# Kernel tuning notes

Hardware: AMD Instinct MI355X
Metric: run time of the kernel (lower is better)

## Reference

```python
import jax, jax.numpy as jnp
import numpy as np

D_MODEL = 768
H = 12
D_K = D_MODEL // H
NEG = -1e9


def setup_inputs() -> dict:
    key = jax.random.key(0)
    ks = jax.random.split(key, 12)
    B, S = 1, 4096
    q = jax.random.normal(ks[0], (B, S, D_MODEL), dtype=jnp.float32)
    k = jax.random.normal(ks[1], (B, S, D_MODEL), dtype=jnp.float32)
    v = jax.random.normal(ks[2], (B, S, D_MODEL), dtype=jnp.float32)
    # causal mask, 1 = attend, 0 = masked (masked_fill on mask == 0)
    mask = jnp.tril(jnp.ones((S, S), dtype=jnp.int32))[None, None, :, :]
    scale = 1.0 / np.sqrt(D_MODEL)
    Wq = jax.random.normal(ks[3], (D_MODEL, D_MODEL), dtype=jnp.float32) * scale
    bq = jnp.zeros((D_MODEL,), dtype=jnp.float32)
    Wk = jax.random.normal(ks[4], (D_MODEL, D_MODEL), dtype=jnp.float32) * scale
    bk = jnp.zeros((D_MODEL,), dtype=jnp.float32)
    Wv = jax.random.normal(ks[5], (D_MODEL, D_MODEL), dtype=jnp.float32) * scale
    bv = jnp.zeros((D_MODEL,), dtype=jnp.float32)
    Wo = jax.random.normal(ks[6], (D_MODEL, D_MODEL), dtype=jnp.float32) * scale
    bo = jnp.zeros((D_MODEL,), dtype=jnp.float32)
    return {"q": q, "k": k, "v": v, "mask": mask,
            "Wq": Wq, "bq": bq, "Wk": Wk, "bk": bk,
            "Wv": Wv, "bv": bv, "Wo": Wo, "bo": bo}


def _split_heads(x):
    B, S, _ = x.shape
    return x.reshape(B, S, H, D_K).transpose(0, 2, 1, 3)  # [B,H,S,Dk]


def reference(q, k, v, mask, Wq, bq, Wk, bk, Wv, bv, Wo, bo):
    # Linear projections (torch Linear: x @ W.T + b; here W stored as [in,out])
    query = _split_heads(q @ Wq + bq)
    key = _split_heads(k @ Wk + bk)
    value = _split_heads(v @ Wv + bv)
    # scaled dot-product attention, full score matrix [B,H,Sq,Sk]
    scores = jnp.einsum("bhqd,bhkd->bhqk", query, key) / jnp.sqrt(
        jnp.asarray(D_K, dtype=query.dtype))
    scores = jnp.where(mask == 0, jnp.asarray(NEG, dtype=scores.dtype), scores)
    attn = jax.nn.softmax(scores, axis=-1)  # dropout p=0.0 -> identity
    x = jnp.einsum("bhqk,bhkd->bhqd", attn, value)
    B, _, S, _ = x.shape
    x = x.transpose(0, 2, 1, 3).reshape(B, S, H * D_K)
    return x @ Wo + bo
```

## Files before the change

### kernel.cpp

```cpp
#include <hip/hip_runtime.h>

typedef __bf16 bf16;
typedef __bf16 bf16x4 __attribute__((ext_vector_type(4)));
typedef __bf16 bf16x8 __attribute__((ext_vector_type(8)));
typedef float  floatx4 __attribute__((ext_vector_type(4)));

#define MFMA16(a,b,c) __builtin_amdgcn_mfma_f32_16x16x32_bf16((a),(b),(c),0,0,0)

static constexpr int S_LEN = 4096;
static constexpr int DM = 768;
static constexpr int NH = 12;
static constexpr int W_ELEMS = 768 * 768;
static constexpr int PARTS_PER_HEAD = 80;

__device__ __forceinline__ void gld16(const bf16* g, bf16* l) {
    __builtin_amdgcn_global_load_lds(
        (const __attribute__((address_space(1))) void*)g,
        (__attribute__((address_space(3))) void*)l, 16, 0, 0);
}

__global__ __launch_bounds__(256) void prep_kernel(
    const float* __restrict__ q, const float* __restrict__ k, const float* __restrict__ v,
    const float* __restrict__ W0, const float* __restrict__ W1,
    const float* __restrict__ W2, const float* __restrict__ W3,
    bf16* Qc, bf16* Kc, bf16* Vc,
    bf16* T0, bf16* T1, bf16* T2, bf16* T3, int n)
{
    const int y = blockIdx.y;
    const int tid = threadIdx.x;
    if (y < 3) {
        const float* src = y == 0 ? q : (y == 1 ? k : v);
        bf16* dst = y == 0 ? Qc : (y == 1 ? Kc : Vc);
        int i = (blockIdx.x * 256 + tid) * 4;
        if (i < n) {
            float4 w = *(const float4*)&src[i];
            bf16x4 o; o[0] = (bf16)w.x; o[1] = (bf16)w.y; o[2] = (bf16)w.z; o[3] = (bf16)w.w;
            *(bf16x4*)&dst[i] = o;
        }
        return;
    }
    int x = blockIdx.x;
    if (x >= 576) return;
    const int mat = x / 144, t = x % 144;
    const float* W = mat == 0 ? W0 : (mat == 1 ? W1 : (mat == 2 ? W2 : W3));
    bf16* T = mat == 0 ? T0 : (mat == 1 ? T1 : (mat == 2 ? T2 : T3));
    const int k0 = (t / 12) * 64, n0 = (t % 12) * 64;
    __shared__ float Tl[64][65];
#pragma unroll
    for (int i = 0; i < 4; ++i) {
        int idx = i * 256 + tid;
        int r = idx >> 4, c4 = idx & 15;
        float4 w = *(const float4*)&W[(k0 + r) * 768 + n0 + c4 * 4];
        Tl[c4 * 4 + 0][r] = w.x; Tl[c4 * 4 + 1][r] = w.y;
        Tl[c4 * 4 + 2][r] = w.z; Tl[c4 * 4 + 3][r] = w.w;
    }
    __syncthreads();
#pragma unroll
    for (int i = 0; i < 4; ++i) {
        int idx = i * 256 + tid;
        int c = idx >> 4, r4 = idx & 15;
        bf16x4 o;
        o[0] = (bf16)Tl[c][r4 * 4 + 0]; o[1] = (bf16)Tl[c][r4 * 4 + 1];
        o[2] = (bf16)Tl[c][r4 * 4 + 2]; o[3] = (bf16)Tl[c][r4 * 4 + 3];
        *(bf16x4*)&T[(n0 + c) * 768 + k0 + r4 * 4] = o;
    }
}

template <bool OUT_F32>
__global__ __launch_bounds__(256) void gemm128_kernel(
    const bf16* __restrict__ A0, const bf16* __restrict__ A1, const bf16* __restrict__ A2,
    const bf16* __restrict__ B0, const bf16* __restrict__ B1, const bf16* __restrict__ B2,
    const float* __restrict__ c0, const float* __restrict__ c1, const float* __restrict__ c2,
    void* O0, void* O1, void* O2, int M, int N, int K)
{
    const int z = blockIdx.z;
    const bf16* A = z == 0 ? A0 : (z == 1 ? A1 : A2);
    const bf16* B = z == 0 ? B0 : (z == 1 ? B1 : B2);
    const float* bias = z == 0 ? c0 : (z == 1 ? c1 : c2);
    void* C = z == 0 ? O0 : (z == 1 ? O1 : O2);

    __shared__ bf16 As[2][128 * 64];
    __shared__ bf16 Bs[2][128 * 64];
    const int tid = threadIdx.x, lane = tid & 63, wave = tid >> 6;
    const int quad = lane >> 4, l16 = lane & 15, l8 = l16 & 7;
    const int rw = wave >> 1, cw = wave & 1;
    const int m0 = blockIdx.x * 128, n0 = blockIdx.y * 128;

    floatx4 acc[4][4] = {};

    auto stage = [&](int kt, int buf) {
#pragma unroll
        for (int i = 0; i < 4; ++i) {
            int ch = i * 256 + tid;
            int m = ch >> 3, kg = ch & 7;
            int kgd = kg ^ (m & 7);
            gld16(A + (size_t)(m0 + m) * K + kt * 64 + kgd * 8, &As[buf][ch * 8]);
        }
#pragma unroll
        for (int i = 0; i < 4; ++i) {
            int ch = i * 256 + tid;
            int n = ch >> 3, kg = ch & 7;
            int kgd = kg ^ (n & 7);
            gld16(B + (size_t)(n0 + n) * K + kt * 64 + kgd * 8, &Bs[buf][ch * 8]);
        }
    };

    const int NT = K >> 6;
    stage(0, 0);
    __syncthreads();

    for (int kt = 0; kt < NT; ++kt) {
        const int cur = kt & 1;
        if (kt + 1 < NT) stage(kt + 1, cur ^ 1);
#pragma unroll
        for (int ks = 0; ks < 2; ++ks) {
            bf16x8 a[4], b[4];
#pragma unroll
            for (int mt = 0; mt < 4; ++mt)
                a[mt] = *(const bf16x8*)&As[cur][(rw * 64 + mt * 16 + l16) * 64 + (((ks * 4 + quad) ^ l8) << 3)];
#pragma unroll
            for (int nt = 0; nt < 4; ++nt)
                b[nt] = *(const bf16x8*)&Bs[cur][(cw * 64 + nt * 16 + l16) * 64 + (((ks * 4 + quad) ^ l8) << 3)];
#pragma unroll
            for (int mt = 0; mt < 4; ++mt)
#pragma unroll
                for (int nt = 0; nt < 4; ++nt)
                    acc[mt][nt] = MFMA16(a[mt], b[nt], acc[mt][nt]);
        }
        __syncthreads();
    }
#pragma unroll
    for (int mt = 0; mt < 4; ++mt) {
        int row = m0 + rw * 64 + mt * 16 + quad * 4;
#pragma unroll
        for (int nt = 0; nt < 4; ++nt) {
            int col = n0 + cw * 64 + nt * 16 + l16;
            float bv = bias[col];
#pragma unroll
            for (int r = 0; r < 4; ++r) {
                float v = acc[mt][nt][r] + bv;
                if (OUT_F32) ((float*)C)[(size_t)(row + r) * N + col] = v;
                else         ((bf16*)C)[(size_t)(row + r) * N + col] = (bf16)v;
            }
        }
    }
}

__global__ __launch_bounds__(256) void attn_kernel(
    const bf16* __restrict__ Q, const bf16* __restrict__ K,
    const bf16* __restrict__ V, float* __restrict__ Opart,
    float* __restrict__ Lpart)
{
    __shared__ bf16 Ps[128 * 64];
    __shared__ bf16 Ks[2][64 * 64];
    __shared__ bf16 Vt[2][64 * 64];

    const int h = blockIdx.y;
    const int idx = PARTS_PER_HEAD - 1 - (int)blockIdx.x;
    int qb, c;
    if (idx < 8)       { qb = idx;                    c = 0;            }
    else if (idx < 24) { qb = 8  + ((idx - 8) >> 1);  c = (idx - 8) & 1; }
    else if (idx < 48) { qb = 16 + (idx - 24) / 3;    c = (idx - 24) % 3; }
    else               { qb = 24 + ((idx - 48) >> 2); c = (idx - 48) & 3; }
    const int jstart = c * 16;
    const int jend0  = 2 * qb + 2;
    const int jend   = (jstart + 16 < jend0) ? jstart + 16 : jend0;

    const int tid = threadIdx.x, lane = tid & 63, wave = tid >> 6;
    const int quad = lane >> 4, l16 = lane & 15, l8 = l16 & 7;
    const int qrow0 = qb * 128;
    const int cb = h * 64;

    auto stageK = [&](int j, int buf) {
#pragma unroll
        for (int i = 0; i < 2; ++i) {
            int ch = i * 256 + tid;
            int row = ch >> 3, kg = ch & 7;
            int kgd = kg ^ (row & 7);
            gld16(K + (size_t)(j * 64 + row) * DM + cb + kgd * 8, &Ks[buf][ch * 8]);
        }
    };
    auto loadV = [&](int j, bf16 vr[2][8]) {
#pragma unroll
        for (int i = 0; i < 2; ++i) {
            int kg = wave + i * 4;
#pragma unroll
            for (int u = 0; u < 8; ++u)
                vr[i][u] = V[(size_t)(j * 64 + kg * 8 + u) * DM + cb + lane];
        }
    };
    auto writeV = [&](int buf, bf16 vr[2][8]) {
#pragma unroll
        for (int i = 0; i < 2; ++i) {
            int kg = wave + i * 4;
            bf16x8 t;
#pragma unroll
            for (int u = 0; u < 8; ++u) t[u] = vr[i][u];
            *(bf16x8*)&Vt[buf][lane * 64 + ((kg ^ (lane & 7)) << 3)] = t;
        }
    };

    bf16x8 qreg[2][2];
#pragma unroll
    for (int mt = 0; mt < 2; ++mt)
#pragma unroll
        for (int ks = 0; ks < 2; ++ks)
            qreg[mt][ks] = *(const bf16x8*)&Q[(size_t)(qrow0 + wave * 32 + mt * 16 + l16) * DM
                                             + cb + ks * 32 + quad * 8];

    stageK(jstart, 0);
    bf16 v0[2][8];
    loadV(jstart, v0);
    writeV(0, v0);
    __syncthreads();

    floatx4 o[2][4] = {};
    float lsum[2][4] = {};
    constexpr float CE = 0.18033688011112042f;

    for (int j = jstart; j < jend; ++j) {
        const int cur = (j - jstart) & 1;
        bf16 vr[2][8];
        if (j + 1 < jend) {
            stageK(j + 1, cur ^ 1);
            loadV(j + 1, vr);
        }

        floatx4 s[2][4] = {};
#pragma unroll
        for (int ks = 0; ks < 2; ++ks) {
            bf16x8 bfr[4];
#pragma unroll
            for (int ct = 0; ct < 4; ++ct)
                bfr[ct] = *(const bf16x8*)&Ks[cur][(ct * 16 + l16) * 64 + (((ks * 4 + quad) ^ l8) << 3)];
#pragma unroll
            for (int mt = 0; mt < 2; ++mt)
#pragma unroll
                for (int ct = 0; ct < 4; ++ct)
                    s[mt][ct] = MFMA16(qreg[mt][ks], bfr[ct], s[mt][ct]);
        }

#pragma unroll
        for (int mt = 0; mt < 2; ++mt) {
            const int rbase = qrow0 + wave * 32 + mt * 16;
            const bool nomask = (j * 64 + 63) <= rbase;
            const int prow0 = wave * 32 + mt * 16 + quad * 4;
#pragma unroll
            for (int ct = 0; ct < 4; ++ct) {
                const int kj = j * 64 + ct * 16 + l16;
#pragma unroll
                for (int r = 0; r < 4; ++r) {
                    float p = __builtin_amdgcn_exp2f(s[mt][ct][r] * CE);
                    if (!nomask && kj > rbase + quad * 4 + r) p = 0.0f;
                    lsum[mt][r] += p;
                    Ps[(prow0 + r) * 64 +
                       (((ct * 2 + (l16 >> 3)) ^ ((quad * 4 + r) & 7)) << 3) + l8] = (bf16)p;
                }
            }
        }

#pragma unroll
        for (int ks = 0; ks < 2; ++ks) {
            bf16x8 bfr[4], afr[2];
#pragma unroll
            for (int ct = 0; ct < 4; ++ct)
                bfr[ct] = *(const bf16x8*)&Vt[cur][(ct * 16 + l16) * 64 + (((ks * 4 + quad) ^ l8) << 3)];
#pragma unroll
            for (int mt = 0; mt < 2; ++mt)
                afr[mt] = *(const bf16x8*)&Ps[(wave * 32 + mt * 16 + l16) * 64 + (((ks * 4 + quad) ^ l8) << 3)];
#pragma unroll
            for (int mt = 0; mt < 2; ++mt)
#pragma unroll
                for (int ct = 0; ct < 4; ++ct)
                    o[mt][ct] = MFMA16(afr[mt], bfr[ct], o[mt][ct]);
        }

        if (j + 1 < jend) writeV(cur ^ 1, vr);
        __syncthreads();
    }

    float* Op = Opart + (size_t)(h * PARTS_PER_HEAD + idx) * 128 * 64;
    float* Lp = Lpart + (size_t)(h * PARTS_PER_HEAD + idx) * 128;
#pragma unroll
    for (int mt = 0; mt < 2; ++mt) {
#pragma unroll
        for (int r = 0; r < 4; ++r) {
            float l = lsum[mt][r];
#pragma unroll
            for (int d = 1; d < 16; d <<= 1) l += __shfl_xor(l, d);
            const int rl = wave * 32 + mt * 16 + quad * 4 + r;
#pragma unroll
            for (int ct = 0; ct < 4; ++ct)
                Op[rl * 64 + ct * 16 + l16] = o[mt][ct][r];
            if (l16 == 0) Lp[rl] = l;
        }
    }
}

__global__ __launch_bounds__(256) void attn_combine_kernel(
    const float* __restrict__ Opart, const float* __restrict__ Lpart,
    bf16* __restrict__ X)
{
    const int qb = blockIdx.x, h = blockIdx.y;
    const int nc = 1 + (qb >> 3);
    const int base = (qb < 8) ? qb
                   : (qb < 16) ? 8 + (qb - 8) * 2
                   : (qb < 24) ? 24 + (qb - 16) * 3
                   : 48 + (qb - 24) * 4;
    const float* Op0 = Opart + (size_t)(h * PARTS_PER_HEAD + base) * 128 * 64;
    const float* Lp0 = Lpart + (size_t)(h * PARTS_PER_HEAD + base) * 128;

    for (int e = threadIdx.x * 4; e < 128 * 64; e += 1024) {
        const int row = e >> 6, col = e & 63;
        float4 acc = {0.f, 0.f, 0.f, 0.f};
        float l = 0.f;
        for (int p = 0; p < nc; ++p) {
            float4 w = *(const float4*)&Op0[p * 128 * 64 + e];
            acc.x += w.x; acc.y += w.y; acc.z += w.z; acc.w += w.w;
            l += Lp0[p * 128 + row];
        }
        const float rl = 1.0f / l;
        bf16x4 ov;
        ov[0] = (bf16)(acc.x * rl); ov[1] = (bf16)(acc.y * rl);
        ov[2] = (bf16)(acc.z * rl); ov[3] = (bf16)(acc.w * rl);
        *(bf16x4*)&X[(size_t)(qb * 128 + row) * DM + h * 64 + col] = ov;
    }
}

extern "C" void kernel_launch(void* const* d_in, const int* in_sizes, int n_in,
                              void* d_out, int out_size, void* d_ws, size_t ws_size,
                              hipStream_t stream)
{
    const float* q  = (const float*)d_in[0];
    const float* k  = (const float*)d_in[1];
    const float* v  = (const float*)d_in[2];
    const float* Wq = (const float*)d_in[4];
    const float* bq = (const float*)d_in[5];
    const float* Wk = (const float*)d_in[6];
    const float* bk = (const float*)d_in[7];
    const float* Wv = (const float*)d_in[8];
    const float* bv = (const float*)d_in[9];
    const float* Wo = (const float*)d_in[10];
    const float* bo = (const float*)d_in[11];

    const size_t NE = (size_t)S_LEN * DM;
    bf16* base = (bf16*)d_ws;
    bf16* Qc = base;
    bf16* Kc = base + NE;
    bf16* Vc = base + 2 * NE;
    bf16* Qp = base + 3 * NE;
    bf16* Kp = base + 4 * NE;
    bf16* Vp = base + 5 * NE;
    bf16* Wt = base + 6 * NE;
    bf16 *Wqt = Wt, *Wkt = Wt + W_ELEMS, *Wvt = Wt + 2 * W_ELEMS, *Wot = Wt + 3 * W_ELEMS;
    float* Opart = (float*)(Wt + 4 * W_ELEMS);
    float* Lpart = Opart + (size_t)NH * PARTS_PER_HEAD * 128 * 64;
    bf16* Xb = Qc;

    prep_kernel<<<dim3(3072, 4), 256, 0, stream>>>(
        q, k, v, Wq, Wk, Wv, Wo, Qc, Kc, Vc, Wqt, Wkt, Wvt, Wot, (int)NE);
    gemm128_kernel<false><<<dim3(32, 6, 3), 256, 0, stream>>>(
        Qc, Kc, Vc, Wqt, Wkt, Wvt, bq, bk, bv, Qp, Kp, Vp, S_LEN, DM, DM);
    attn_kernel<<<dim3(PARTS_PER_HEAD, NH), 256, 0, stream>>>(Qp, Kp, Vp, Opart, Lpart);
    attn_combine_kernel<<<dim3(32, NH), 256, 0, stream>>>(Opart, Lpart, Xb);
    gemm128_kernel<true><<<dim3(32, 6, 1), 256, 0, stream>>>(
        Xb, Xb, Xb, Wot, Wot, Wot, bo, bo, bo, d_out, d_out, d_out, S_LEN, DM, DM);
}
```

Measured before the change: 280.7 us.

## Compute transposed attention scores, fold softmax scale into Q projection, single-buffer V

The QK^T MFMA now computes S^T by swapping operands, so each lane holds four consecutive key columns for one query row. The P tile is then written to LDS as packed bf16x4 stores, and the row sum becomes a per-lane accumulator reduced with two shuffles. The softmax scale (1/sqrt(d)·log2e) is moved into the Q projection GEMM epilogue, which removes a multiply per score. V is now single-buffered in LDS, with an extra barrier around its write, to cut LDS use. The risk is that the added barriers reduce overlap, and pre-scaled bf16 Q changes rounding slightly.

Result: faster. 268.9 us (-4.2%).

```diff
diff --git a/kernel.cpp b/kernel.cpp
--- a/kernel.cpp
+++ b/kernel.cpp
@@ -12,6 +12,7 @@
 static constexpr int NH = 12;
 static constexpr int W_ELEMS = 768 * 768;
 static constexpr int PARTS_PER_HEAD = 80;
+static constexpr float CE = 0.18033688011112042f;
 
 __device__ __forceinline__ void gld16(const bf16* g, bf16* l) {
     __builtin_amdgcn_global_load_lds(
@@ -71,13 +72,14 @@
     const bf16* __restrict__ A0, const bf16* __restrict__ A1, const bf16* __restrict__ A2,
     const bf16* __restrict__ B0, const bf16* __restrict__ B1, const bf16* __restrict__ B2,
     const float* __restrict__ c0, const float* __restrict__ c1, const float* __restrict__ c2,
-    void* O0, void* O1, void* O2, int M, int N, int K)
+    void* O0, void* O1, void* O2, int M, int N, int K, float qscale)
 {
     const int z = blockIdx.z;
     const bf16* A = z == 0 ? A0 : (z == 1 ? A1 : A2);
     const bf16* B = z == 0 ? B0 : (z == 1 ? B1 : B2);
     const float* bias = z == 0 ? c0 : (z == 1 ? c1 : c2);
     void* C = z == 0 ? O0 : (z == 1 ? O1 : O2);
+    const float osc = (z == 0) ? qscale : 1.0f;
 
     __shared__ bf16 As[2][128 * 64];
     __shared__ bf16 Bs[2][128 * 64];
@@ -138,7 +140,7 @@
             float bv = bias[col];
 #pragma unroll
             for (int r = 0; r < 4; ++r) {
-                float v = acc[mt][nt][r] + bv;
+                float v = (acc[mt][nt][r] + bv) * osc;
                 if (OUT_F32) ((float*)C)[(size_t)(row + r) * N + col] = v;
                 else         ((bf16*)C)[(size_t)(row + r) * N + col] = (bf16)v;
             }
@@ -153,7 +155,7 @@
 {
     __shared__ bf16 Ps[128 * 64];
     __shared__ bf16 Ks[2][64 * 64];
-    __shared__ bf16 Vt[2][64 * 64];
+    __shared__ bf16 Vt[64 * 64];
 
     const int h = blockIdx.y;
     const int idx = PARTS_PER_HEAD - 1 - (int)blockIdx.x;
@@ -189,14 +191,14 @@
                 vr[i][u] = V[(size_t)(j * 64 + kg * 8 + u) * DM + cb + lane];
         }
     };
-    auto writeV = [&](int buf, bf16 vr[2][8]) {
+    auto writeV = [&](bf16 vr[2][8]) {
 #pragma unroll
         for (int i = 0; i < 2; ++i) {
             int kg = wave + i * 4;
             bf16x8 t;
 #pragma unroll
             for (int u = 0; u < 8; ++u) t[u] = vr[i][u];
-            *(bf16x8*)&Vt[buf][lane * 64 + ((kg ^ (lane & 7)) << 3)] = t;
+            *(bf16x8*)&Vt[lane * 64 + ((kg ^ (lane & 7)) << 3)] = t;
         }
     };
 
@@ -211,12 +213,14 @@
     stageK(jstart, 0);
     bf16 v0[2][8];
     loadV(jstart, v0);
-    writeV(0, v0);
+    writeV(v0);
     __syncthreads();
 
     floatx4 o[2][4] = {};
-    float lsum[2][4] = {};
-    constexpr float CE = 0.18033688011112042f;
+    float lsum[2] = {0.f, 0.f};
+    const int prowbase = (wave * 32 + l16) * 64;
+    const int psub = (quad & 1) * 4;
+    const int c16base = (quad >> 1);
 
     for (int j = jstart; j < jend; ++j) {
         const int cur = (j - jstart) & 1;
@@ -226,37 +230,52 @@
             loadV(j + 1, vr);
         }
 
-        floatx4 s[2][4] = {};
+        floatx4 st[2][4] = {};
 #pragma unroll
         for (int ks = 0; ks < 2; ++ks) {
-            bf16x8 bfr[4];
+            bf16x8 kfr[4];
 #pragma unroll
             for (int ct = 0; ct < 4; ++ct)
-                bfr[ct] = *(const bf16x8*)&Ks[cur][(ct * 16 + l16) * 64 + (((ks * 4 + quad) ^ l8) << 3)];
+                kfr[ct] = *(const bf16x8*)&Ks[cur][(ct * 16 + l16) * 64 + (((ks * 4 + quad) ^ l8) << 3)];
 #pragma unroll
             for (int mt = 0; mt < 2; ++mt)
 #pragma unroll
                 for (int ct = 0; ct < 4; ++ct)
-                    s[mt][ct] = MFMA16(qreg[mt][ks], bfr[ct], s[mt][ct]);
+                    st[mt][ct] = MFMA16(kfr[ct], qreg[mt][ks], st[mt][ct]);
         }
 
 #pragma unroll
         for (int mt = 0; mt < 2; ++mt) {
-            const int rbase = qrow0 + wave * 32 + mt * 16;
-            const bool nomask = (j * 64 + 63) <= rbase;
-            const int prow0 = wave * 32 + mt * 16 + quad * 4;
-#pragma unroll
-            for (int ct = 0; ct < 4; ++ct) {
-                const int kj = j * 64 + ct * 16 + l16;
-#pragma unroll
-                for (int r = 0; r < 4; ++r) {
-                    float p = __builtin_amdgcn_exp2f(s[mt][ct][r] * CE);
-                    if (!nomask && kj > rbase + quad * 4 + r) p = 0.0f;
-                    lsum[mt][r] += p;
-                    Ps[(prow0 + r) * 64 +
-                       (((ct * 2 + (l16 >> 3)) ^ ((quad * 4 + r) & 7)) << 3) + l8] = (bf16)p;
+            const int qs0 = qrow0 + wave * 32 + mt * 16;
+            const int pb = prowbase + mt * 16 * 64;
+            float lp = 0.f;
+            if ((j * 64 + 63) <= qs0) {
+#pragma unroll
+                for (int ct = 0; ct < 4; ++ct) {
+                    bf16x4 pk;
+#pragma unroll
+                    for (int r = 0; r < 4; ++r) {
+                        float p = __builtin_amdgcn_exp2f(st[mt][ct][r]);
+                        lp += p; pk[r] = (bf16)p;
+                    }
+                    *(bf16x4*)&Ps[pb + ((((ct * 2 + c16base) ^ l8) << 3) + psub)] = pk;
+                }
+            } else {
+                const int qg = qs0 + l16;
+#pragma unroll
+                for (int ct = 0; ct < 4; ++ct) {
+                    const int kg0 = j * 64 + ct * 16 + quad * 4;
+                    bf16x4 pk;
+#pragma unroll
+                    for (int r = 0; r < 4; ++r) {
+                        float p = (kg0 + r > qg) ? 0.f
+                                  : __builtin_amdgcn_exp2f(st[mt][ct][r]);
+                        lp += p; pk[r] = (bf16)p;
+                    }
+                    *(bf16x4*)&Ps[pb + ((((ct * 2 + c16base) ^ l8) << 3) + psub)] = pk;
                 }
             }
+            lsum[mt] += lp;
         }
 
 #pragma unroll
@@ -264,7 +283,7 @@
             bf16x8 bfr[4], afr[2];
 #pragma unroll
             for (int ct = 0; ct < 4; ++ct)
-                bfr[ct] = *(const bf16x8*)&Vt[cur][(ct * 16 + l16) * 64 + (((ks * 4 + quad) ^ l8) << 3)];
+                bfr[ct] = *(const bf16x8*)&Vt[(ct * 16 + l16) * 64 + (((ks * 4 + quad) ^ l8) << 3)];
 #pragma unroll
             for (int mt = 0; mt < 2; ++mt)
                 afr[mt] = *(const bf16x8*)&Ps[(wave * 32 + mt * 16 + l16) * 64 + (((ks * 4 + quad) ^ l8) << 3)];
@@ -275,24 +294,27 @@
                     o[mt][ct] = MFMA16(afr[mt], bfr[ct], o[mt][ct]);
         }
 
-        if (j + 1 < jend) writeV(cur ^ 1, vr);
-        __syncthreads();
+        if (j + 1 < jend) {
+            __syncthreads();
+            writeV(vr);
+            __syncthreads();
+        }
     }
 
     float* Op = Opart + (size_t)(h * PARTS_PER_HEAD + idx) * 128 * 64;
     float* Lp = Lpart + (size_t)(h * PARTS_PER_HEAD + idx) * 128;
 #pragma unroll
     for (int mt = 0; mt < 2; ++mt) {
+        float l = lsum[mt];
+        l += __shfl_xor(l, 16);
+        l += __shfl_xor(l, 32);
+        if (lane < 16) Lp[wave * 32 + mt * 16 + l16] = l;
 #pragma unroll
         for (int r = 0; r < 4; ++r) {
-            float l = lsum[mt][r];
-#pragma unroll
-            for (int d = 1; d < 16; d <<= 1) l += __shfl_xor(l, d);
             const int rl = wave * 32 + mt * 16 + quad * 4 + r;
 #pragma unroll
             for (int ct = 0; ct < 4; ++ct)
                 Op[rl * 64 + ct * 16 + l16] = o[mt][ct][r];
-            if (l16 == 0) Lp[rl] = l;
         }
     }
 }
@@ -360,9 +382,9 @@
     prep_kernel<<<dim3(3072, 4), 256, 0, stream>>>(
         q, k, v, Wq, Wk, Wv, Wo, Qc, Kc, Vc, Wqt, Wkt, Wvt, Wot, (int)NE);
     gemm128_kernel<false><<<dim3(32, 6, 3), 256, 0, stream>>>(
-        Qc, Kc, Vc, Wqt, Wkt, Wvt, bq, bk, bv, Qp, Kp, Vp, S_LEN, DM, DM);
+        Qc, Kc, Vc, Wqt, Wkt, Wvt, bq, bk, bv, Qp, Kp, Vp, S_LEN, DM, DM, CE);
     attn_kernel<<<dim3(PARTS_PER_HEAD, NH), 256, 0, stream>>>(Qp, Kp, Vp, Opart, Lpart);
     attn_combine_kernel<<<dim3(32, NH), 256, 0, stream>>>(Opart, Lpart, Xb);
     gemm128_kernel<true><<<dim3(32, 6, 1), 256, 0, stream>>>(
-        Xb, Xb, Xb, Wot, Wot, Wot, bo, bo, bo, d_out, d_out, d_out, S_LEN, DM, DM);
-}
+        Xb, Xb, Xb, Wot, Wot, Wot, bo, bo, bo, d_out, d_out, d_out, S_LEN, DM, DM, 1.0f);
+}
```
